# Kernel optimization log

Hardware: AMD Instinct MI355X
Metric: run time of the kernel (lower is better)

## Reference

```python
import jax, jax.numpy as jnp
from jax import lax
import numpy as np

GAMMA = 1.0
BIG = 1e10  # stands in for +inf; exp(-BIG/gamma) == 0 in fp32, safe under autodiff


def cosine_distance_matrix(x, y):
    # x: [B,N,d], y: [B,M,d] -> D: [B,N,M] = 1 - cos(x_i, y_j)
    xn = x / (jnp.linalg.norm(x, axis=-1, keepdims=True) + 1e-8)
    yn = y / (jnp.linalg.norm(y, axis=-1, keepdims=True) + 1e-8)
    return 1.0 - jnp.einsum('bnd,bmd->bnm', xn, yn)


def soft_dtw(D, gamma):
    # D: [B,N,M]. Returns R[:, N, M] of the soft-DTW DP:
    # R[i,j] = D[i-1,j-1] + softmin(R[i-1,j-1], R[i-1,j], R[i,j-1])
    B, N, M = D.shape
    # column j=0: R[:,0,0]=0, R[:,i,0]=inf for i>=1  -> shape [B, N+1]
    init_col = jnp.concatenate([jnp.zeros((B, 1), D.dtype),
                                jnp.full((B, N), BIG, D.dtype)], axis=1)

    def col_step(prev_col, d_col):
        # prev_col: R[:, 0:N+1, j-1]  [B, N+1];  d_col: D[:, :, j-1]  [B, N]
        def row_step(carry, inp):
            r_diag, r_up, d = inp  # each [B]: R[i-1,j-1], R[i-1,j]... (see below)
            stacked = jnp.stack([r_diag, carry, r_up], axis=0)  # [3,B]
            softmin = -gamma * jax.nn.logsumexp(-stacked / gamma, axis=0)
            r = d + softmin
            return r, r
        # per-row inputs along i=1..N: diag=prev_col[i-1], up-in-column=prev_col[i]
        inputs = (prev_col[:, :-1].T, prev_col[:, 1:].T, d_col.T)  # each [N,B]
        _, rows = lax.scan(row_step, jnp.full((B,), BIG, D.dtype), inputs)
        new_col = jnp.concatenate([jnp.full((B, 1), BIG, D.dtype), rows.T], axis=1)
        return new_col, None

    final_col, _ = lax.scan(col_step, init_col, jnp.transpose(D, (2, 0, 1)))
    return final_col[:, -1]  # R[:, N, M]


def setup_inputs() -> dict:
    key = jax.random.key(0)
    k1, k2 = jax.random.split(key)
    B, N, M, d = 16, 1024, 1024, 128
    x = jax.random.normal(k1, (B, N, d), dtype=jnp.float32)
    y = jax.random.normal(k2, (B, M, d), dtype=jnp.float32)
    return {"x": x, "y": y}


def reference(x, y):
    D = cosine_distance_matrix(x, y)
    return soft_dtw(D, GAMMA)  # [B]
```

## Files before the change

kernel.cpp:

```cpp
#include <hip/hip_runtime.h>
#include <hip/hip_fp16.h>

#define BATCH 16
#define NROW 1024
#define MCOL 1024
#define DFEAT 128

#define R_DP 16
#define C_DP 8
#define NCH (MCOL / C_DP)
#define NPH_C 191
#define PSTRIDE 194

#define L2E 1.4426950408889634f
#define LN2 0.6931471805599453f

typedef __attribute__((ext_vector_type(8))) short short8;
typedef __attribute__((ext_vector_type(4))) float f32x4;

__device__ inline unsigned short f2bf(float f) {
  unsigned u = __float_as_uint(f);
  return (unsigned short)((u + 0x7fff + ((u >> 16) & 1)) >> 16);
}

__global__ __launch_bounds__(256) void norm_kernel(
    const float* __restrict__ x, const float* __restrict__ y,
    unsigned short* __restrict__ xnb, unsigned short* __restrict__ ynb) {
  int row = blockIdx.x * 4 + (threadIdx.x >> 6);
  int lane = threadIdx.x & 63;
  const float* src;
  unsigned short* dst;
  if (row < BATCH * NROW) {
    src = x + (size_t)row * DFEAT;
    dst = xnb + (size_t)row * DFEAT;
  } else {
    int r2 = row - BATCH * NROW;
    src = y + (size_t)r2 * DFEAT;
    dst = ynb + (size_t)r2 * DFEAT;
  }
  float2 v = *(const float2*)(src + lane * 2);
  float s = v.x * v.x + v.y * v.y;
  #pragma unroll
  for (int o = 32; o > 0; o >>= 1) s += __shfl_xor(s, o, 64);
  float inv = 1.0f / (sqrtf(s) + 1e-8f);
  unsigned short b0 = f2bf(v.x * inv), b1 = f2bf(v.y * inv);
  *(unsigned*)(dst + lane * 2) = (unsigned)b0 | ((unsigned)b1 << 16);
}

__global__ __launch_bounds__(256) void dist_kernel(
    const unsigned short* __restrict__ xnb, const unsigned short* __restrict__ ynb,
    __half* __restrict__ Dphase) {
  __shared__ __align__(16) unsigned char xsb[128 * 256];
  __shared__ __align__(16) unsigned char ysb[128 * 256];

  int b = blockIdx.z, ti0 = blockIdx.y, tj0 = blockIdx.x;
  int I0 = ti0 * 128, J0 = tj0 * 128;
  int tid = threadIdx.x;

  const uint4* xsrc = (const uint4*)(xnb + (size_t)(b * NROW + I0) * DFEAT);
  const uint4* ysrc = (const uint4*)(ynb + (size_t)(b * MCOL + J0) * DFEAT);
  #pragma unroll
  for (int it = 0; it < 8; ++it) {
    int idx = tid + it * 256;
    int row = idx >> 4, cb = (idx & 15) * 16;
    int swz = row * 256 + (cb ^ ((row & 7) << 4));
    *(uint4*)&xsb[swz] = xsrc[idx];
    *(uint4*)&ysb[swz] = ysrc[idx];
  }
  __syncthreads();

  int wid = tid >> 6, lane = tid & 63;
  int wi = wid >> 1, wj = wid & 1;
  int lr = lane & 15, lk = lane >> 4;

  f32x4 acc[4][4] = {};
  #pragma unroll
  for (int ks = 0; ks < 4; ++ks) {
    int cb = ks * 64 + lk * 16;
    short8 af[4], bf[4];
    #pragma unroll
    for (int ti = 0; ti < 4; ++ti) {
      int row = wi * 64 + ti * 16 + lr;
      af[ti] = *(short8*)&xsb[row * 256 + (cb ^ ((row & 7) << 4))];
    }
    #pragma unroll
    for (int tj = 0; tj < 4; ++tj) {
      int row = wj * 64 + tj * 16 + lr;
      bf[tj] = *(short8*)&ysb[row * 256 + (cb ^ ((row & 7) << 4))];
    }
    #pragma unroll
    for (int ti = 0; ti < 4; ++ti)
      #pragma unroll
      for (int tj = 0; tj < 4; ++tj)
        acc[ti][tj] = __builtin_amdgcn_mfma_f32_16x16x32_bf16(
            af[ti], bf[tj], acc[ti][tj], 0, 0, 0);
  }

  #pragma unroll
  for (int ti = 0; ti < 4; ++ti) {
    int gi0 = I0 + wi * 64 + ti * 16;
    int l = gi0 >> 4;
    #pragma unroll
    for (int tj = 0; tj < 4; ++tj) {
      int gj = J0 + wj * 64 + tj * 16 + lr;
      int c = gj >> 3, k = gj & 7;
      int p = c + l;
      #pragma unroll
      for (int v = 0; v < 4; ++v) {
        int r = lk * 4 + v;
        float d = 1.0f - acc[ti][tj][v];
        size_t off = ((((size_t)b * PSTRIDE + p) * R_DP + r) * 64 + l) * C_DP + k;
        Dphase[off] = __float2half(exp2f(-d * L2E));
      }
    }
  }
}


#define MIXMUL_LO(A, h, s) \
  asm("v_fma_mix_f32 %0, %1, %2, %3 op_sel_hi:[1,0,0]" : "=v"(A) : "v"(h), "v"(s), "v"(fzero))
#define MIXMUL_HI(A, h, s) \
  asm("v_fma_mix_f32 %0, %1, %2, %3 op_sel:[1,0,0] op_sel_hi:[1,0,0]" : "=v"(A) : "v"(h), "v"(s), "v"(fzero))
#define MIXFMA_LO(lf, h, a) \
  asm("v_fma_mix_f32 %0, %1, %2, %3 op_sel_hi:[1,0,0]" : "=v"(lf) : "v"(h), "v"(lf), "v"(a))
#define MIXFMA_HI(lf, h, a) \
  asm("v_fma_mix_f32 %0, %1, %2, %3 op_sel:[1,0,0] op_sel_hi:[1,0,0]" : "=v"(lf) : "v"(h), "v"(lf), "v"(a))

__device__ __forceinline__ float shup(float x, bool edge) {
  int xi = __float_as_int(x);
  int sh = __builtin_amdgcn_update_dpp(xi, xi, 0x111, 0xF, 0xF, false);
  int bc = __builtin_amdgcn_update_dpp(xi, xi, 0x142, 0xF, 0xF, false);
  return __int_as_float(edge ? bc : sh);
}

template<bool GUARDED>
__device__ __forceinline__ void dtw_phase_l(int c, int t, bool edge,
    const uint4 (*slot)[64], float* carry, float (&B)[9], float& O, float fzero) {
  float U[9];
  #pragma unroll
  for (int k = 0; k < 9; ++k) U[k] = shup(B[k], edge);
  float Oin = shup(O, edge);
  if (t == 0) {
    #pragma unroll
    for (int k = 0; k < 9; ++k) U[k] = 0.0f;
    if (GUARDED && c == 0) U[0] = 1.0f;
    Oin = O;
  }
  bool act = GUARDED ? ((unsigned)c < 128u) : true;
  if (act) {
    if (GUARDED && c == 0) O = Oin;
    float sc = exp2f((O - Oin) * L2E);
    #pragma unroll
    for (int k = 0; k < 9; ++k) U[k] *= sc;

    #pragma unroll
    for (int r = 0; r < R_DP; ++r) {
      uint4 d = slot[r][t];
      unsigned dw[4] = {d.x, d.y, d.z, d.w};
      float S[8], A[8];
      #pragma unroll
      for (int k = 0; k < 8; ++k) S[k] = U[k] + U[k + 1];
      #pragma unroll
      for (int q = 0; q < 4; ++q) {
        MIXMUL_LO(A[2 * q],     dw[q], S[2 * q]);
        MIXMUL_HI(A[2 * q + 1], dw[q], S[2 * q + 1]);
      }
      float oldc = carry[r], lf = oldc;
      float V[8];
      #pragma unroll
      for (int q = 0; q < 4; ++q) {
        MIXFMA_LO(lf, dw[q], A[2 * q]);     V[2 * q] = lf;
        MIXFMA_HI(lf, dw[q], A[2 * q + 1]); V[2 * q + 1] = lf;
      }
      U[0] = oldc;
      #pragma unroll
      for (int k = 1; k <= 8; ++k) U[k] = V[k - 1];
      carry[r] = lf;
    }

    float rep = carry[R_DP - 1];
    int ex = (int)((__float_as_uint(rep) >> 23) & 0xFF) - 127;
    if ((ex < -20 || ex > 12) && ex < 128) {
      float s = __uint_as_float((unsigned)(127 - ex) << 23);
      #pragma unroll
      for (int r = 0; r < R_DP; ++r) carry[r] *= s;
      #pragma unroll
      for (int k = 0; k < 9; ++k) U[k] *= s;
      O -= (float)ex * LN2;
    }
    #pragma unroll
    for (int k = 0; k < 9; ++k) B[k] = U[k];
  }
}

#define GL(Lr, SB, OFF) \
  asm volatile("global_load_dwordx4 %0, %1, %2 offset:" OFF : "=v"(Lr) : "v"(voff), "s"(SB));

#define ISSUE16(L, S0, S1, S2, S3)                               \
  GL(L[0],  S0, "0")    GL(L[1],  S0, "1024")                    \
  GL(L[2],  S0, "2048") GL(L[3],  S0, "3072")                    \
  GL(L[4],  S1, "0")    GL(L[5],  S1, "1024")                    \
  GL(L[6],  S1, "2048") GL(L[7],  S1, "3072")                    \
  GL(L[8],  S2, "0")    GL(L[9],  S2, "1024")                    \
  GL(L[10], S2, "2048") GL(L[11], S2, "3072")                    \
  GL(L[12], S3, "0")    GL(L[13], S3, "1024")                    \
  GL(L[14], S3, "2048") GL(L[15], S3, "3072")

#define WRSLOT(SLOT, L)                                          \
  _Pragma("unroll")                                              \
  for (int r = 0; r < R_DP; ++r) ring[SLOT][r][t] = L[r];

__global__ __launch_bounds__(128, 1) void dtw_kernel(
    const __half* __restrict__ Dphase, float* __restrict__ out) {
  __shared__ __align__(16) uint4 ring[4][R_DP][64];
  __shared__ volatile unsigned prodCnt, consCnt;

  int b = blockIdx.x;
  int tid = threadIdx.x;
  int w = __builtin_amdgcn_readfirstlane(tid >> 6);
  int t = tid & 63;
  float fzero = 0.0f;
  int voff = t * 16;

  if (tid == 0) { prodCnt = 0; consCnt = 0; }
  __syncthreads();

  const char* g = (const char*)Dphase + (size_t)b * PSTRIDE * 16384;

  if (w == 1) {
    uint4 A[R_DP], Bb[R_DP];
    {
      const char* s0 = g;
      const char* s1 = g + 4096;
      const char* s2 = g + 8192;
      const char* s3 = g + 12288;
      if ((unsigned)(0 - t) < 128u) { ISSUE16(A, s0, s1, s2, s3) }
    }
    for (int p = 0; p < 192; p += 2) {
      {
        int pn = (p + 1 > 190) ? 190 : p + 1;
        const char* s0 = g + ((size_t)pn << 14);
        const char* s1 = s0 + 4096;
        const char* s2 = s0 + 8192;
        const char* s3 = s0 + 12288;
        if ((unsigned)(pn - t) < 128u) { ISSUE16(Bb, s0, s1, s2, s3) }
        asm volatile("s_waitcnt vmcnt(16)" ::: "memory");
        __builtin_amdgcn_sched_barrier(0);
        while ((int)(p - (int)consCnt) >= 4) __builtin_amdgcn_s_sleep(8);
        if ((unsigned)(p - t) < 128u) { WRSLOT(p & 3, A) }
        asm volatile("s_waitcnt lgkmcnt(0)" ::: "memory");
        if (t == 0) prodCnt = p + 1;
      }
      {
        int pn = (p + 2 > 190) ? 190 : p + 2;
        const char* s0 = g + ((size_t)pn << 14);
        const char* s1 = s0 + 4096;
        const char* s2 = s0 + 8192;
        const char* s3 = s0 + 12288;
        if ((unsigned)(pn - t) < 128u) { ISSUE16(A, s0, s1, s2, s3) }
        asm volatile("s_waitcnt vmcnt(16)" ::: "memory");
        __builtin_amdgcn_sched_barrier(0);
        while ((int)((p + 1) - (int)consCnt) >= 4) __builtin_amdgcn_s_sleep(8);
        if ((unsigned)((p + 1) - t) < 128u) { WRSLOT((p + 1) & 3, Bb) }
        asm volatile("s_waitcnt lgkmcnt(0)" ::: "memory");
        if (t == 0) prodCnt = p + 2;
      }
    }
    asm volatile("s_waitcnt vmcnt(0)" ::: "memory");
  } else {
    const bool edge = (t != 0) && ((t & 15) == 0);
    float carry[R_DP];
    #pragma unroll
    for (int r = 0; r < R_DP; ++r) carry[r] = 0.0f;
    float B[9] = {};
    float O = 0.0f;

    #define CONSUME(P, G)                                                    \
      {                                                                      \
        while ((int)prodCnt < (P) + 1) __builtin_amdgcn_s_sleep(2);          \
        asm volatile("s_waitcnt lgkmcnt(0)" ::: "memory");                   \
        __builtin_amdgcn_sched_barrier(0);                                   \
        dtw_phase_l<G>((P) - t, t, edge, ring[(P) & 3], carry, B, O, fzero); \
        asm volatile("s_waitcnt lgkmcnt(0)" ::: "memory");                   \
        if (t == 0) consCnt = (P) + 1;                                       \
      }

    for (int p = 0; p < 64; ++p)    CONSUME(p, true)
    for (int p = 64; p < 128; ++p)  CONSUME(p, false)
    for (int p = 128; p < 191; ++p) CONSUME(p, true)

    if (t == 63) out[b] = O - logf(carry[R_DP - 1]);
    #undef CONSUME
  }
}

extern "C" void kernel_launch(void* const* d_in, const int* in_sizes, int n_in,
                              void* d_out, int out_size, void* d_ws, size_t ws_size,
                              hipStream_t stream) {
  const float* x = (const float*)d_in[0];
  const float* y = (const float*)d_in[1];
  float* out = (float*)d_out;

  char* ws = (char*)d_ws;
  __half* Dphase = (__half*)ws;
  size_t dp_bytes = (size_t)BATCH * PSTRIDE * 16384;
  unsigned short* xnb = (unsigned short*)(ws + dp_bytes);
  unsigned short* ynb = xnb + (size_t)BATCH * NROW * DFEAT;

  norm_kernel<<<(2 * BATCH * NROW) / 4, 256, 0, stream>>>(x, y, xnb, ynb);
  dist_kernel<<<dim3(MCOL / 128, NROW / 128, BATCH), 256, 0, stream>>>(
      xnb, ynb, Dphase);
  dtw_kernel<<<BATCH, 128, 0, stream>>>(Dphase, out);
}
```

Before: 286.2 us.

## Split DTW producer into two wavefronts each loading half the rows

The single producer wavefront that streamed 16 rows of phase data per step into the LDS ring is replaced by two producer wavefronts. Each loads 8 rows with its own progress flag, and the consumer waits on both flags. This halves the outstanding loads and registers per producer and is meant to keep the serial DP consumer from stalling on data. The rescale step also gains a positivity guard on the representative value, which is a small correctness or robustness change. The cost is an extra wavefront per block and a second flag to poll.

```diff
diff --git a/kernel.cpp b/kernel.cpp
--- a/kernel.cpp
+++ b/kernel.cpp
@@ -9,7 +9,6 @@
 #define R_DP 16
 #define C_DP 8
 #define NCH (MCOL / C_DP)
-#define NPH_C 191
 #define PSTRIDE 194
 
 #define L2E 1.4426950408889634f
@@ -179,94 +178,88 @@
     }
 
     float rep = carry[R_DP - 1];
-    int ex = (int)((__float_as_uint(rep) >> 23) & 0xFF) - 127;
-    if ((ex < -20 || ex > 12) && ex < 128) {
-      float s = __uint_as_float((unsigned)(127 - ex) << 23);
-      #pragma unroll
-      for (int r = 0; r < R_DP; ++r) carry[r] *= s;
-      #pragma unroll
-      for (int k = 0; k < 9; ++k) U[k] *= s;
-      O -= (float)ex * LN2;
+    if (rep > 0.0f) {
+      int ex = (int)((__float_as_uint(rep) >> 23) & 0xFF) - 127;
+      if ((ex < -20 || ex > 12) && ex < 128) {
+        float s = __uint_as_float((unsigned)(127 - ex) << 23);
+        #pragma unroll
+        for (int r = 0; r < R_DP; ++r) carry[r] *= s;
+        #pragma unroll
+        for (int k = 0; k < 9; ++k) U[k] *= s;
+        O -= (float)ex * LN2;
+      }
     }
     #pragma unroll
     for (int k = 0; k < 9; ++k) B[k] = U[k];
   }
 }
 
-#define GL(Lr, SB, OFF) \
+#define GLP(Lr, SB, OFF) \
   asm volatile("global_load_dwordx4 %0, %1, %2 offset:" OFF : "=v"(Lr) : "v"(voff), "s"(SB));
 
-#define ISSUE16(L, S0, S1, S2, S3)                               \
-  GL(L[0],  S0, "0")    GL(L[1],  S0, "1024")                    \
-  GL(L[2],  S0, "2048") GL(L[3],  S0, "3072")                    \
-  GL(L[4],  S1, "0")    GL(L[5],  S1, "1024")                    \
-  GL(L[6],  S1, "2048") GL(L[7],  S1, "3072")                    \
-  GL(L[8],  S2, "0")    GL(L[9],  S2, "1024")                    \
-  GL(L[10], S2, "2048") GL(L[11], S2, "3072")                    \
-  GL(L[12], S3, "0")    GL(L[13], S3, "1024")                    \
-  GL(L[14], S3, "2048") GL(L[15], S3, "3072")
-
-#define WRSLOT(SLOT, L)                                          \
-  _Pragma("unroll")                                              \
-  for (int r = 0; r < R_DP; ++r) ring[SLOT][r][t] = L[r];
-
-__global__ __launch_bounds__(128, 1) void dtw_kernel(
+#define ISSUE8(L, S0, S1)                                        \
+  GLP(L[0], S0, "0")    GLP(L[1], S0, "1024")                    \
+  GLP(L[2], S0, "2048") GLP(L[3], S0, "3072")                    \
+  GLP(L[4], S1, "0")    GLP(L[5], S1, "1024")                    \
+  GLP(L[6], S1, "2048") GLP(L[7], S1, "3072")
+
+#define PSTEP(PH, CUR, NXT)                                                  \
+  {                                                                          \
+    int pn = (PH) + 1 > 190 ? 190 : (PH) + 1;                                \
+    const char* s0 = base + ((size_t)pn << 14);                              \
+    const char* s1 = s0 + 4096;                                              \
+    if ((unsigned)(pn - t) < 128u) { ISSUE8(NXT, s0, s1) }                   \
+    asm volatile("s_waitcnt vmcnt(8)" ::: "memory");                         \
+    __builtin_amdgcn_sched_barrier(0);                                       \
+    while ((int)((PH) - (int)*cc) >= 4) __builtin_amdgcn_s_sleep(8);         \
+    if ((unsigned)((PH) - t) < 128u) {                                       \
+      _Pragma("unroll")                                                      \
+      for (int r = 0; r < 8; ++r) ring[(PH) & 3][RS + r][t] = CUR[r];        \
+    }                                                                        \
+    asm volatile("s_waitcnt lgkmcnt(0)" ::: "memory");                       \
+    if (t == 0) *myflag = (PH) + 1;                                          \
+  }
+
+__device__ __forceinline__ void producer(const char* g, int t, int RS,
+    volatile unsigned* myflag, volatile unsigned* cc,
+    uint4 (*ring)[R_DP][64]) {
+  int voff = t * 16;
+  const char* base = g + RS * 1024;
+
+  uint4 A[8], Bb[8];
+  {
+    const char* s0 = base;
+    const char* s1 = base + 4096;
+    if ((unsigned)(0 - t) < 128u) { ISSUE8(A, s0, s1) }
+  }
+  for (int p = 0; p < 192; p += 2) {
+    PSTEP(p, A, Bb)
+    PSTEP(p + 1, Bb, A)
+  }
+  asm volatile("s_waitcnt vmcnt(0)" ::: "memory");
+}
+
+__global__ __launch_bounds__(192, 1) void dtw_kernel(
     const __half* __restrict__ Dphase, float* __restrict__ out) {
   __shared__ __align__(16) uint4 ring[4][R_DP][64];
-  __shared__ volatile unsigned prodCnt, consCnt;
+  __shared__ volatile unsigned pc[2];
+  __shared__ volatile unsigned cc;
 
   int b = blockIdx.x;
   int tid = threadIdx.x;
   int w = __builtin_amdgcn_readfirstlane(tid >> 6);
   int t = tid & 63;
   float fzero = 0.0f;
-  int voff = t * 16;
-
-  if (tid == 0) { prodCnt = 0; consCnt = 0; }
+
+  if (tid == 0) { pc[0] = 0; pc[1] = 0; cc = 0; }
   __syncthreads();
 
   const char* g = (const char*)Dphase + (size_t)b * PSTRIDE * 16384;
 
   if (w == 1) {
-    uint4 A[R_DP], Bb[R_DP];
-    {
-      const char* s0 = g;
-      const char* s1 = g + 4096;
-      const char* s2 = g + 8192;
-      const char* s3 = g + 12288;
-      if ((unsigned)(0 - t) < 128u) { ISSUE16(A, s0, s1, s2, s3) }
-    }
-    for (int p = 0; p < 192; p += 2) {
-      {
-        int pn = (p + 1 > 190) ? 190 : p + 1;
-        const char* s0 = g + ((size_t)pn << 14);
-        const char* s1 = s0 + 4096;
-        const char* s2 = s0 + 8192;
-        const char* s3 = s0 + 12288;
-        if ((unsigned)(pn - t) < 128u) { ISSUE16(Bb, s0, s1, s2, s3) }
-        asm volatile("s_waitcnt vmcnt(16)" ::: "memory");
-        __builtin_amdgcn_sched_barrier(0);
-        while ((int)(p - (int)consCnt) >= 4) __builtin_amdgcn_s_sleep(8);
-        if ((unsigned)(p - t) < 128u) { WRSLOT(p & 3, A) }
-        asm volatile("s_waitcnt lgkmcnt(0)" ::: "memory");
-        if (t == 0) prodCnt = p + 1;
-      }
-      {
-        int pn = (p + 2 > 190) ? 190 : p + 2;
-        const char* s0 = g + ((size_t)pn << 14);
-        const char* s1 = s0 + 4096;
-        const char* s2 = s0 + 8192;
-        const char* s3 = s0 + 12288;
-        if ((unsigned)(pn - t) < 128u) { ISSUE16(A, s0, s1, s2, s3) }
-        asm volatile("s_waitcnt vmcnt(16)" ::: "memory");
-        __builtin_amdgcn_sched_barrier(0);
-        while ((int)((p + 1) - (int)consCnt) >= 4) __builtin_amdgcn_s_sleep(8);
-        if ((unsigned)((p + 1) - t) < 128u) { WRSLOT((p + 1) & 3, Bb) }
-        asm volatile("s_waitcnt lgkmcnt(0)" ::: "memory");
-        if (t == 0) prodCnt = p + 2;
-      }
-    }
-    asm volatile("s_waitcnt vmcnt(0)" ::: "memory");
+    producer(g, t, 0, &pc[0], &cc, ring);
+  } else if (w == 2) {
+    producer(g, t, 8, &pc[1], &cc, ring);
   } else {
     const bool edge = (t != 0) && ((t & 15) == 0);
     float carry[R_DP];
@@ -277,12 +270,13 @@
 
     #define CONSUME(P, G)                                                    \
       {                                                                      \
-        while ((int)prodCnt < (P) + 1) __builtin_amdgcn_s_sleep(2);          \
+        while ((int)pc[0] < (P) + 1 || (int)pc[1] < (P) + 1)                 \
+          __builtin_amdgcn_s_sleep(2);                                       \
         asm volatile("s_waitcnt lgkmcnt(0)" ::: "memory");                   \
         __builtin_amdgcn_sched_barrier(0);                                   \
         dtw_phase_l<G>((P) - t, t, edge, ring[(P) & 3], carry, B, O, fzero); \
         asm volatile("s_waitcnt lgkmcnt(0)" ::: "memory");                   \
-        if (t == 0) consCnt = (P) + 1;                                       \
+        if (t == 0) cc = (P) + 1;                                            \
       }
 
     for (int p = 0; p < 64; ++p)    CONSUME(p, true)
@@ -310,5 +304,5 @@
   norm_kernel<<<(2 * BATCH * NROW) / 4, 256, 0, stream>>>(x, y, xnb, ynb);
   dist_kernel<<<dim3(MCOL / 128, NROW / 128, BATCH), 256, 0, stream>>>(
       xnb, ynb, Dphase);
-  dtw_kernel<<<BATCH, 128, 0, stream>>>(Dphase, out);
-}
+  dtw_kernel<<<BATCH, 192, 0, stream>>>(Dphase, out);
+}
```

New measurement: 312.0 us. 9.0% more time.
